# Kernel optimization log

Measured on AMD Instinct MI355X. Metric: run time of the kernel, lower is better.

The kernel has to match this reference:

```python
import jax, jax.numpy as jnp
import numpy as np

IMAGE_SIZE = (1024, 1024)
STRIDE = 16
RATIOS = (0.5, 1.0, 2.0)
SCALES = (8, 16, 32)
NUM_PRE_NMS = 6000
NUM_POST_NMS = 300
NMS_THRESH = 0.7
FEATURE_DEPTH = 512
RPN_DEPTH = 512
NUM_ANCHOR = len(RATIOS) * len(SCALES)


def _generate_anchors():
    # Faithful replication of RPN.__generate_anchors__ (numpy, at trace time).
    yloc = np.arange(STRIDE / 2, IMAGE_SIZE[0], STRIDE).astype(int)
    xloc = np.arange(STRIDE / 2, IMAGE_SIZE[1], STRIDE).astype(int)
    ctrs = np.array(np.meshgrid(xloc, yloc)).T.reshape(-1, 2)
    dims = [[STRIDE * s * np.sqrt(r), STRIDE * s * np.sqrt(1.0 / r)] for s in SCALES for r in RATIOS]
    blocks = []
    for d in dims:
        d = np.asarray(d)
        blocks.append(np.concatenate([ctrs - 0.5 * d, ctrs + 0.5 * d], axis=1))
    return np.concatenate(blocks, axis=0).astype(np.float32)  # (K*H*W, 4)

ANCHORS = _generate_anchors()


def conv2d(x, w, b, pad):
    y = jax.lax.conv_general_dilated(
        x, w, window_strides=(1, 1), padding=((pad, pad), (pad, pad)),
        dimension_numbers=('NCHW', 'OIHW', 'NCHW'))
    return y + b[None, :, None, None]


def nms_single(boxes, scores):
    # boxes: (A,4) yxyx, scores: (A,). Greedy NMS, jit-compatible.
    sc, idx = jax.lax.top_k(scores, NUM_PRE_NMS)
    b = boxes[idx]  # (P,4)
    y1, x1, y2, x2 = b[:, 0], b[:, 1], b[:, 2], b[:, 3]
    areas = (y2 - y1) * (x2 - x1)

    def body(i, carry):
        s, picked = carry
        j = jnp.argmax(s)
        picked = picked.at[i].set(j)
        bb = b[j]
        yy1 = jnp.maximum(bb[0], y1)
        xx1 = jnp.maximum(bb[1], x1)
        yy2 = jnp.minimum(bb[2], y2)
        xx2 = jnp.minimum(bb[3], x2)
        inter = jnp.maximum(yy2 - yy1, 0.0) * jnp.maximum(xx2 - xx1, 0.0)
        iou = inter / (areas[j] + areas - inter + 1e-9)
        s = jnp.where(iou >= NMS_THRESH, -jnp.inf, s)  # suppresses j itself (iou=1)
        return (s, picked)

    _, picked = jax.lax.fori_loop(0, NUM_POST_NMS, body, (sc, jnp.zeros((NUM_POST_NMS,), jnp.int32)))
    return b[picked]  # (POST, 4)


def rpn_forward(features, conv_w, conv_b, cls_w, cls_b, bbox_w, bbox_b):
    B, C, H, W = features.shape
    rpn = jax.nn.relu(conv2d(features, conv_w, conv_b, 1))
    # Objectness
    cls = conv2d(rpn, cls_w, cls_b, 0)  # (B, 2K, H, W)
    score = jnp.transpose(cls, (0, 2, 3, 1)).reshape(B, H, W, NUM_ANCHOR, 2)
    prob = jax.nn.softmax(score, axis=-1)[..., 1].reshape(B, -1)  # (B, A)
    score = score.reshape(B, -1, 2)
    tgt = conv2d(rpn, bbox_w, bbox_b, 0)  # (B, 4K, H, W)
    tgt = jnp.transpose(tgt, (0, 2, 3, 1)).reshape(B, -1, 4)
    # Decode targets against anchors (targets2box): (dy,dx,dh,dw) vs centre/hw anchors
    a = jnp.asarray(ANCHORS)
    ah = a[:, 2] - a[:, 0]
    aw = a[:, 3] - a[:, 1]
    acy = a[:, 0] + 0.5 * ah
    acx = a[:, 1] + 0.5 * aw
    dy, dx, dh, dw = tgt[..., 0], tgt[..., 1], tgt[..., 2], tgt[..., 3]
    pcy = acy + dy * ah
    pcx = acx + dx * aw
    ph = ah * jnp.exp(dh)
    pw = aw * jnp.exp(dw)
    boxes = jnp.stack([pcy - 0.5 * ph, pcx - 0.5 * pw, pcy + 0.5 * ph, pcx + 0.5 * pw], axis=-1)
    lim = jnp.array([IMAGE_SIZE[0] - 1, IMAGE_SIZE[1] - 1, IMAGE_SIZE[0] - 1, IMAGE_SIZE[1] - 1], boxes.dtype)
    boxes = jnp.clip(boxes, 0.0, lim)
    top = jax.vmap(nms_single)(boxes, prob)  # (B, POST, 4)
    return jnp.floor(top), score, tgt


def setup_inputs() -> dict:
    key = jax.random.key(0)
    ks = jax.random.split(key, 7)
    B, H, W = 8, IMAGE_SIZE[0] // STRIDE, IMAGE_SIZE[1] // STRIDE
    std = 0.01  # normal_init(mean=0, std=0.01) convention for RPN heads
    return {
        'features': jax.random.normal(ks[0], (B, FEATURE_DEPTH, H, W), jnp.float32),
        'conv_w': std * jax.random.normal(ks[1], (RPN_DEPTH, FEATURE_DEPTH, 3, 3), jnp.float32),
        'conv_b': jnp.zeros((RPN_DEPTH,), jnp.float32),
        'cls_w': std * jax.random.normal(ks[2], (NUM_ANCHOR * 2, RPN_DEPTH, 1, 1), jnp.float32),
        'cls_b': jnp.zeros((NUM_ANCHOR * 2,), jnp.float32),
        'bbox_w': std * jax.random.normal(ks[3], (NUM_ANCHOR * 4, RPN_DEPTH, 1, 1), jnp.float32),
        'bbox_b': jnp.zeros((NUM_ANCHOR * 4,), jnp.float32),
    }


def reference(features, conv_w, conv_b, cls_w, cls_b, bbox_w, bbox_b):
    return rpn_forward(features, conv_w, conv_b, cls_w, cls_b, bbox_w, bbox_b)
```

## Files before the change

### kernel.cpp

```cpp
#include <hip/hip_runtime.h>
#include <math.h>
#include <stdint.h>

typedef unsigned long long u64;

#define NANCH 36864
#define PRE_NMS 6000
#define POST_NMS 300

#define OFF_WT    0ull
#define OFF_KEYS  9437184ull
#define OFF_BOX   11796480ull
#define OFF_CAND  16515072ull
#define OFF_META  17039360ull
#define OFF_RPN   17039488ull

#define SCORE_OFF 9600u
#define TGT_OFF   599424u

__global__ void wt_kernel(const float* __restrict__ w, float* __restrict__ wt) {
    int idx = blockIdx.x * 256 + threadIdx.x;
    if (idx >= 9 * 512 * 512) return;
    int co = idx & 511;
    int ci = (idx >> 9) & 511;
    int tap = idx >> 18;
    wt[idx] = w[(size_t)(co * 512 + ci) * 9 + tap];
}

#define FS_CI6 432
#define FS_TOT6 3456
#define WS64 4608

__global__ __launch_bounds__(256, 2) void conv64(const float* __restrict__ F,
                                                 const float* __restrict__ Wt,
                                                 const float* __restrict__ bias,
                                                 float* __restrict__ rpn,
                                                 int b_base) {
    __shared__ __align__(16) float Fs[2][FS_TOT6];
    __shared__ __align__(16) float Ws[2][WS64];
    int t = threadIdx.x;
    int cg = t >> 5;
    int pg = t & 31;
    int rp = pg >> 4;
    int x0 = (pg & 15) << 2;
    int y0 = blockIdx.x << 2;
    int co0 = blockIdx.y * 64;
    int bl = blockIdx.z;
    const float* Fb = F + (size_t)(b_base + bl) * 512 * 4096;

    int rmap[6]; int nv = 0;
#pragma unroll
    for (int rr = 0; rr < 6; ++rr) {
        int gy = y0 + rr - 1;
        if (gy >= 0 && gy < 64) rmap[nv++] = rr;
    }
    int nF = (8 * 16) * nv;
    int fG[3], fL[3]; bool fV[3];
#pragma unroll
    for (int k = 0; k < 3; ++k) {
        int item = t + (k << 8);
        bool ok = item < nF;
        fV[k] = ok;
        int per_ci = nv << 4;
        int ci = ok ? (item / per_ci) : 0;
        int rem = item - ci * per_ci;
        if (!ok) rem = 0;
        int rv = rem >> 4;
        int f4 = rem & 15;
        int rr = rmap[rv];
        int gy = y0 + rr - 1;
        fG[k] = ci * 4096 + gy * 64 + (f4 << 2);
        fL[k] = ci * FS_CI6 + rr * 72 + 1 + (f4 << 2);
    }
    int wG[5], wL[5]; bool wV[5];
#pragma unroll
    for (int k = 0; k < 5; ++k) {
        int i4 = t + (k << 8);
        bool ok = i4 < 1152;
        wV[k] = ok;
        int idx = ok ? (i4 << 2) : 0;
        int ci = idx / 576;
        int rem = idx - ci * 576;
        int tap = rem >> 6;
        int co = rem & 63;
        wG[k] = tap * (512 * 512) + ci * 512 + co;
        wL[k] = idx;
    }
    float4 z4 = make_float4(0.f, 0.f, 0.f, 0.f);
    for (int i = t; i < (2 * FS_TOT6) / 4; i += 256) ((float4*)Fs)[i] = z4;

    float acc[8][2][4];
#pragma unroll
    for (int c2 = 0; c2 < 8; ++c2)
#pragma unroll
        for (int r = 0; r < 2; ++r)
#pragma unroll
            for (int j = 0; j < 4; ++j) acc[c2][r][j] = 0.f;

    float4 fQ[3], wQ[5];
#pragma unroll
    for (int k = 0; k < 3; ++k) fQ[k] = fV[k] ? *(const float4*)&Fb[fG[k]] : z4;
#pragma unroll
    for (int k = 0; k < 5; ++k) wQ[k] = wV[k] ? *(const float4*)&Wt[co0 + wG[k]] : z4;
#pragma unroll
    for (int k = 0; k < 3; ++k)
        if (fV[k]) {
            float* p = &Fs[0][fL[k]];
            p[0] = fQ[k].x; p[1] = fQ[k].y; p[2] = fQ[k].z; p[3] = fQ[k].w;
        }
#pragma unroll
    for (int k = 0; k < 5; ++k)
        if (wV[k]) *(float4*)&Ws[0][wL[k]] = wQ[k];
    {
        const float* Fn = Fb + 8 * 4096;
        const float* Wn = Wt + 8 * 512 + co0;
#pragma unroll
        for (int k = 0; k < 3; ++k) fQ[k] = fV[k] ? *(const float4*)&Fn[fG[k]] : z4;
#pragma unroll
        for (int k = 0; k < 5; ++k) wQ[k] = wV[k] ? *(const float4*)&Wn[wG[k]] : z4;
    }
    for (int c = 0; c < 64; ++c) {
        int cur = c & 1;
        int alt = cur ^ 1;
        __syncthreads();
        if (c + 1 < 64) {
#pragma unroll
            for (int k = 0; k < 3; ++k)
                if (fV[k]) {
                    float* p = &Fs[alt][fL[k]];
                    p[0] = fQ[k].x; p[1] = fQ[k].y; p[2] = fQ[k].z; p[3] = fQ[k].w;
                }
#pragma unroll
            for (int k = 0; k < 5; ++k)
                if (wV[k]) *(float4*)&Ws[alt][wL[k]] = wQ[k];
        }
        if (c + 2 < 64) {
            const float* Fn = Fb + (size_t)(c + 2) * 8 * 4096;
            const float* Wn = Wt + (size_t)(c + 2) * 8 * 512 + co0;
#pragma unroll
            for (int k = 0; k < 3; ++k) fQ[k] = fV[k] ? *(const float4*)&Fn[fG[k]] : z4;
#pragma unroll
            for (int k = 0; k < 5; ++k) wQ[k] = wV[k] ? *(const float4*)&Wn[wG[k]] : z4;
        }
#pragma unroll 1
        for (int ci = 0; ci < 8; ++ci) {
            float vv[4][6];
#pragma unroll
            for (int r2 = 0; r2 < 4; ++r2) {
                int base = ci * FS_CI6 + ((rp << 1) + r2) * 72 + x0;
                float4 a4 = *(float4*)&Fs[cur][base];
                float2 a2 = *(float2*)&Fs[cur][base + 4];
                vv[r2][0] = a4.x; vv[r2][1] = a4.y; vv[r2][2] = a4.z;
                vv[r2][3] = a4.w; vv[r2][4] = a2.x; vv[r2][5] = a2.y;
            }
#pragma unroll
            for (int tap = 0; tap < 9; ++tap) {
                int dy = tap / 3;
                int dx = tap % 3;
                int wb = ci * 576 + tap * 64 + cg * 8;
                float4 wa = *(float4*)&Ws[cur][wb];
                float4 wbv = *(float4*)&Ws[cur][wb + 4];
                float wv[8] = {wa.x, wa.y, wa.z, wa.w, wbv.x, wbv.y, wbv.z, wbv.w};
#pragma unroll
                for (int c2 = 0; c2 < 8; ++c2)
#pragma unroll
                    for (int r = 0; r < 2; ++r)
#pragma unroll
                        for (int j = 0; j < 4; ++j)
                            acc[c2][r][j] += wv[c2] * vv[r + dy][j + dx];
            }
        }
    }
#pragma unroll
    for (int c2 = 0; c2 < 8; ++c2) {
        int co = co0 + cg * 8 + c2;
        float bs = bias[co];
#pragma unroll
        for (int r = 0; r < 2; ++r) {
            int ry = y0 + (rp << 1) + r;
            float4 o;
            o.x = fmaxf(acc[c2][r][0] + bs, 0.f);
            o.y = fmaxf(acc[c2][r][1] + bs, 0.f);
            o.z = fmaxf(acc[c2][r][2] + bs, 0.f);
            o.w = fmaxf(acc[c2][r][3] + bs, 0.f);
            *(float4*)&rpn[(size_t)(bl * 512 + co) * 4096 + ry * 64 + x0] = o;
        }
    }
}

__global__ __launch_bounds__(512) void heads_lds(const float* __restrict__ rpn,
                                                 const float* __restrict__ cls_w,
                                                 const float* __restrict__ cls_b,
                                                 const float* __restrict__ bbox_w,
                                                 const float* __restrict__ bbox_b,
                                                 float* __restrict__ out,
                                                 u64* __restrict__ keys,
                                                 int b_base) {
    __shared__ float rT[64][64];
    __shared__ float wT[54][64];
    __shared__ float outS[54][64];
    int t = threadIdx.x;
    int px = t & 63;
    int g = t >> 6;
    int y = blockIdx.x;
    int bl = blockIdx.y;
    int b = b_base + bl;
    int nch = (g < 6) ? 7 : 6;

    float acc[7];
#pragma unroll
    for (int m = 0; m < 7; ++m) acc[m] = 0.f;

    for (int c8 = 0; c8 < 8; ++c8) {
#pragma unroll
        for (int i = 0; i < 2; ++i) {
            int f4 = t + (i << 9);
            int ci = f4 >> 4;
            int c4 = (f4 & 15) << 2;
            *(float4*)&rT[ci][c4] =
                *(const float4*)&rpn[((size_t)(bl * 512 + c8 * 64 + ci)) * 4096 + y * 64 + c4];
        }
#pragma unroll
        for (int i = 0; i < 2; ++i) {
            int f4 = t + (i << 9);
            if (f4 < 864) {
                int ch = f4 >> 4;
                int c4 = (f4 & 15) << 2;
                const float* src = (ch < 18)
                                       ? &cls_w[(size_t)ch * 512 + c8 * 64 + c4]
                                       : &bbox_w[(size_t)(ch - 18) * 512 + c8 * 64 + c4];
                *(float4*)&wT[ch][c4] = *(const float4*)src;
            }
        }
        __syncthreads();
        for (int ci = 0; ci < 64; ++ci) {
            float rv = rT[ci][px];
#pragma unroll
            for (int m = 0; m < 7; ++m) {
                if (m < nch) acc[m] += wT[g + (m << 3)][ci] * rv;
            }
        }
        __syncthreads();
    }
#pragma unroll
    for (int m = 0; m < 7; ++m) {
        if (m < nch) {
            int ch = g + (m << 3);
            float bs = (ch < 18) ? cls_b[ch] : bbox_b[ch - 18];
            outS[ch][px] = acc[m] + bs;
        }
    }
    __syncthreads();

    for (int fl = t; fl < 54 * 64; fl += 512) {
        int ch = fl >> 6;
        int p2 = fl & 63;
        float v = outS[ch][p2];
        size_t i0 = (size_t)(y * 64 + p2) * 9;
        if (ch < 18) {
            out[SCORE_OFF + ((size_t)b * NANCH + i0 + (ch >> 1)) * 2 + (ch & 1)] = v;
        } else {
            int c2 = ch - 18;
            out[TGT_OFF + ((size_t)b * NANCH + i0 + (c2 >> 2)) * 4 + (c2 & 3)] = v;
        }
    }
    for (int fl = t; fl < 9 * 64; fl += 512) {
        int a = fl >> 6;
        int p2 = fl & 63;
        float s0 = outS[a * 2][p2];
        float s1 = outS[a * 2 + 1][p2];
        float mm = fmaxf(s0, s1);
        float e0 = expf(s0 - mm);
        float e1 = expf(s1 - mm);
        float pr = e1 / (e0 + e1);
        int idx = (y * 64 + p2) * 9 + a;
        keys[(size_t)b * NANCH + idx] =
            ((u64)__float_as_uint(pr) << 32) | (u64)(0xFFFFFFFFu - (unsigned)idx);
    }
}

__global__ void box_kernel(const float* __restrict__ out, float* __restrict__ box) {
    int b = blockIdx.y;
    int i = blockIdx.x * 256 + threadIdx.x;
    const float* tg = &out[TGT_OFF + ((size_t)b * NANCH + i) * 4];
    float dyv = tg[0], dxv = tg[1], dhv = tg[2], dwv = tg[3];
    int dim = i >> 12, rem = i & 4095;
    double cxd = (double)(8 + 16 * (rem >> 6));
    double cyd = (double)(8 + 16 * (rem & 63));
    const double sca[3] = {8.0, 16.0, 32.0};
    const double rat[3] = {0.5, 1.0, 2.0};
    double sc = sca[dim / 3], ra = rat[dim % 3];
    double d0 = 16.0 * sc * sqrt(ra);
    double d1 = 16.0 * sc * sqrt(1.0 / ra);
    float a0 = (float)(cxd - 0.5 * d0);
    float a1 = (float)(cyd - 0.5 * d1);
    float a2 = (float)(cxd + 0.5 * d0);
    float a3 = (float)(cyd + 0.5 * d1);
    float ah = __fsub_rn(a2, a0), aw = __fsub_rn(a3, a1);
    float acy = __fadd_rn(a0, __fmul_rn(0.5f, ah));
    float acx = __fadd_rn(a1, __fmul_rn(0.5f, aw));
    float pcy = __fadd_rn(acy, __fmul_rn(dyv, ah));
    float pcx = __fadd_rn(acx, __fmul_rn(dxv, aw));
    float ph = __fmul_rn(ah, expf(dhv));
    float pw = __fmul_rn(aw, expf(dwv));
    float q0 = fminf(fmaxf(__fsub_rn(pcy, __fmul_rn(0.5f, ph)), 0.f), 1023.f);
    float q1 = fminf(fmaxf(__fsub_rn(pcx, __fmul_rn(0.5f, pw)), 0.f), 1023.f);
    float q2 = fminf(fmaxf(__fadd_rn(pcy, __fmul_rn(0.5f, ph)), 0.f), 1023.f);
    float q3 = fminf(fmaxf(__fadd_rn(pcx, __fmul_rn(0.5f, pw)), 0.f), 1023.f);
    *(float4*)&box[((size_t)b * NANCH + i) * 4] = make_float4(q0, q1, q2, q3);
}

__global__ __launch_bounds__(256) void select_kernel(const u64* __restrict__ keys,
                                                     u64* __restrict__ metaT,
                                                     unsigned* __restrict__ ctr) {
    __shared__ unsigned hist[256];
    __shared__ u64 sh_prefix;
    __shared__ unsigned sh_r;
    int b = blockIdx.x, t = threadIdx.x;
    if (t == 0) { sh_prefix = 0ull; sh_r = PRE_NMS; }
    __syncthreads();
    for (int round = 0; round < 8; ++round) {
        int shift = 56 - 8 * round;
        hist[t] = 0u;
        __syncthreads();
        u64 prefix = sh_prefix;
        for (int i = t; i < NANCH; i += 256) {
            u64 k = keys[(size_t)b * NANCH + i];
            bool ok = (round == 0) || ((k >> (shift + 8)) == prefix);
            if (ok) atomicAdd(&hist[(unsigned)(k >> shift) & 255u], 1u);
        }
        __syncthreads();
        if (t == 0) {
            unsigned r = sh_r, acc = 0;
            int digit = 0;
            for (int bin = 255; bin >= 0; --bin) {
                unsigned c = hist[bin];
                if (acc + c >= r) { digit = bin; sh_r = r - acc; break; }
                acc += c;
            }
            sh_prefix = (prefix << 8) | (u64)digit;
        }
        __syncthreads();
    }
    if (t == 0) {
        metaT[b] = sh_prefix;
        ctr[b] = 0u;
    }
}

__global__ void gather_kernel(const u64* __restrict__ keys, const u64* __restrict__ metaT,
                              unsigned* __restrict__ ctr, u64* __restrict__ candK) {
    int b = blockIdx.y;
    int i = blockIdx.x * 256 + threadIdx.x;
    u64 T = metaT[b];
    u64 k = keys[(size_t)b * NANCH + i];
    if (k >= T) {
        unsigned pos = atomicAdd(&ctr[b], 1u);
        if (pos < 8192u) candK[(size_t)b * 8192 + pos] = k;
    }
}

__global__ __launch_bounds__(512) void sortc_kernel(u64* __restrict__ candK) {
    __shared__ u64 K[8192];
    int b = blockIdx.x, t = threadIdx.x;
    for (int i = t; i < 8192; i += 512)
        K[i] = (i < PRE_NMS) ? candK[(size_t)b * 8192 + i] : 0ull;
    __syncthreads();
    for (int k = 2; k <= 8192; k <<= 1) {
        for (int j = k >> 1; j > 0; j >>= 1) {
            for (int i = t; i < 8192; i += 512) {
                int l = i ^ j;
                if (l > i) {
                    u64 a = K[i], c = K[l];
                    bool up = ((i & k) == 0);
                    bool sw = up ? (a < c) : (a > c);
                    if (sw) { K[i] = c; K[l] = a; }
                }
            }
            __syncthreads();
        }
    }
    for (int i = t; i < 8192; i += 512)
        candK[(size_t)b * 8192 + i] = K[i];
}

__global__ __launch_bounds__(256) void nms_scan(const u64* __restrict__ candK,
                                                const float* __restrict__ box,
                                                float* __restrict__ out_top) {
    __shared__ float kb0[POST_NMS], kb1[POST_NMS], kb2[POST_NMS], kb3[POST_NMS],
        kar[POST_NMS];
    __shared__ u64 mask[4];
    __shared__ float cand0[4];
    int b = blockIdx.x, t = threadIdx.x;
    int w = t >> 6, lane = t & 63;

    float c0[24], c1[24], c2[24], c3[24], ar[24];
    bool alv[24];
#pragma unroll
    for (int m = 0; m < 24; ++m) {
        int q = m * 256 + t;
        u64 kk = (q < PRE_NMS) ? candK[(size_t)b * 8192 + q] : 0ull;
        alv[m] = (kk != 0ull);
        if (alv[m]) {
            unsigned idx = 0xFFFFFFFFu - (unsigned)(kk & 0xFFFFFFFFull);
            const float* bp = &box[((size_t)b * NANCH + idx) * 4];
            c0[m] = bp[0]; c1[m] = bp[1]; c2[m] = bp[2]; c3[m] = bp[3];
        } else {
            c0[m] = c1[m] = c2[m] = c3[m] = 0.f;
        }
        ar[m] = __fmul_rn(__fsub_rn(c2[m], c0[m]), __fsub_rn(c3[m], c1[m]));
    }
    if (t == 0) { cand0[0] = c0[0]; cand0[1] = c1[0]; cand0[2] = c2[0]; cand0[3] = c3[0]; }

    int K = 0;
    bool done = false;
    for (int m = 0; m < 24 && !done; ++m) {
        bool a = alv[m];
        float C0 = c0[m], C1 = c1[m], C2 = c2[m], C3 = c3[m], AR = ar[m];
        for (int k = 0; k < K; ++k) {
            float yy1 = fmaxf(kb0[k], C0);
            float xx1 = fmaxf(kb1[k], C1);
            float yy2 = fminf(kb2[k], C2);
            float xx2 = fminf(kb3[k], C3);
            float inter = __fmul_rn(fmaxf(__fsub_rn(yy2, yy1), 0.f),
                                    fmaxf(__fsub_rn(xx2, xx1), 0.f));
            float denom = __fadd_rn(__fsub_rn(__fadd_rn(kar[k], AR), inter), 1e-9f);
            if (__fdiv_rn(inter, denom) >= 0.7f) a = false;
        }
        __syncthreads();
        u64 bal = __ballot(a);
        if (lane == 0) mask[w] = bal;
        __syncthreads();
        while (true) {
            int L = -1;
#pragma unroll
            for (int ww = 0; ww < 4; ++ww)
                if (L < 0 && mask[ww] != 0ull) L = ww * 64 + (__ffsll(mask[ww]) - 1);
            if (L < 0) break;
            if (t == L) {
                kb0[K] = C0; kb1[K] = C1; kb2[K] = C2; kb3[K] = C3; kar[K] = AR;
            }
            __syncthreads();
            float P0 = kb0[K], P1 = kb1[K], P2 = kb2[K], P3 = kb3[K], AP = kar[K];
            if (a) {
                float yy1 = fmaxf(P0, C0);
                float xx1 = fmaxf(P1, C1);
                float yy2 = fminf(P2, C2);
                float xx2 = fminf(P3, C3);
                float inter = __fmul_rn(fmaxf(__fsub_rn(yy2, yy1), 0.f),
                                        fmaxf(__fsub_rn(xx2, xx1), 0.f));
                float denom = __fadd_rn(__fsub_rn(__fadd_rn(AP, AR), inter), 1e-9f);
                if (__fdiv_rn(inter, denom) >= 0.7f) a = false;
            }
            K++;
            if (K == POST_NMS) done = true;
            u64 bal2 = __ballot(a);
            if (lane == 0) mask[w] = bal2;
            __syncthreads();
            if (done) break;
        }
    }
    __syncthreads();
    for (int i = t; i < POST_NMS; i += 256) {
        float o0, o1, o2, o3;
        if (i < K) { o0 = kb0[i]; o1 = kb1[i]; o2 = kb2[i]; o3 = kb3[i]; }
        else       { o0 = cand0[0]; o1 = cand0[1]; o2 = cand0[2]; o3 = cand0[3]; }
        float* o = out_top + ((size_t)b * POST_NMS + i) * 4;
        o[0] = floorf(o0); o[1] = floorf(o1); o[2] = floorf(o2); o[3] = floorf(o3);
    }
}

extern "C" void kernel_launch(void* const* d_in, const int* in_sizes, int n_in,
                              void* d_out, int out_size, void* d_ws, size_t ws_size,
                              hipStream_t stream) {
    (void)in_sizes; (void)n_in; (void)out_size; (void)ws_size;
    const float* features = (const float*)d_in[0];
    const float* conv_w = (const float*)d_in[1];
    const float* conv_b = (const float*)d_in[2];
    const float* cls_w = (const float*)d_in[3];
    const float* cls_b = (const float*)d_in[4];
    const float* bbox_w = (const float*)d_in[5];
    const float* bbox_b = (const float*)d_in[6];
    float* out = (float*)d_out;
    char* ws = (char*)d_ws;

    float* Wt = (float*)(ws + OFF_WT);
    u64* keys = (u64*)(ws + OFF_KEYS);
    float* box = (float*)(ws + OFF_BOX);
    u64* candK = (u64*)(ws + OFF_CAND);
    u64* metaT = (u64*)(ws + OFF_META);
    unsigned* ctr = (unsigned*)(ws + OFF_META + 64);
    float* rpn = (float*)(ws + OFF_RPN);

    wt_kernel<<<9216, 256, 0, stream>>>(conv_w, Wt);
    for (int h = 0; h < 2; ++h) {
        int b_base = h * 4;
        conv64<<<dim3(16, 8, 4), 256, 0, stream>>>(features, Wt, conv_b, rpn, b_base);
        heads_lds<<<dim3(64, 4), 512, 0, stream>>>(rpn, cls_w, cls_b, bbox_w, bbox_b,
                                                   out, keys, b_base);
    }
    box_kernel<<<dim3(144, 8), 256, 0, stream>>>(out, box);
    select_kernel<<<8, 256, 0, stream>>>(keys, metaT, ctr);
    gather_kernel<<<dim3(144, 8), 256, 0, stream>>>(keys, metaT, ctr, candK);
    sortc_kernel<<<8, 512, 0, stream>>>(candK);
    nms_scan<<<8, 256, 0, stream>>>(candK, box, out);
}
```

Before: 2.520 ms.

## Single-buffer conv LDS and launch all batches at once when workspace allows

The conv kernel drops its double-buffered shared memory for one buffer, with a register prefetch of the next chunk stored after a second barrier. This halves LDS use and removes the launch_bounds hint, so more blocks may fit per CU. When the workspace is large enough, the conv and heads kernels now run over all 8 images in one launch instead of two halves, giving a larger grid and fewer launches. The cost is an extra barrier per channel chunk and less overlap between loads and compute.

```diff
diff --git a/kernel.cpp b/kernel.cpp
--- a/kernel.cpp
+++ b/kernel.cpp
@@ -14,6 +14,8 @@
 #define OFF_CAND  16515072ull
 #define OFF_META  17039360ull
 #define OFF_RPN   17039488ull
+#define IMG_BYTES 8388608ull
+#define WS_NEED8  84148352ull
 
 #define SCORE_OFF 9600u
 #define TGT_OFF   599424u
@@ -31,13 +33,13 @@
 #define FS_TOT6 3456
 #define WS64 4608
 
-__global__ __launch_bounds__(256, 2) void conv64(const float* __restrict__ F,
-                                                 const float* __restrict__ Wt,
-                                                 const float* __restrict__ bias,
-                                                 float* __restrict__ rpn,
-                                                 int b_base) {
-    __shared__ __align__(16) float Fs[2][FS_TOT6];
-    __shared__ __align__(16) float Ws[2][WS64];
+__global__ void conv64s(const float* __restrict__ F,
+                        const float* __restrict__ Wt,
+                        const float* __restrict__ bias,
+                        float* __restrict__ rpn,
+                        int b_base) {
+    __shared__ __align__(16) float Fs[FS_TOT6];
+    __shared__ __align__(16) float Ws[WS64];
     int t = threadIdx.x;
     int cg = t >> 5;
     int pg = t & 31;
@@ -87,7 +89,7 @@
         wL[k] = idx;
     }
     float4 z4 = make_float4(0.f, 0.f, 0.f, 0.f);
-    for (int i = t; i < (2 * FS_TOT6) / 4; i += 256) ((float4*)Fs)[i] = z4;
+    for (int i = t; i < FS_TOT6 / 4; i += 256) ((float4*)Fs)[i] = z4;
 
     float acc[8][2][4];
 #pragma unroll
@@ -105,38 +107,18 @@
 #pragma unroll
     for (int k = 0; k < 3; ++k)
         if (fV[k]) {
-            float* p = &Fs[0][fL[k]];
+            float* p = &Fs[fL[k]];
             p[0] = fQ[k].x; p[1] = fQ[k].y; p[2] = fQ[k].z; p[3] = fQ[k].w;
         }
 #pragma unroll
     for (int k = 0; k < 5; ++k)
-        if (wV[k]) *(float4*)&Ws[0][wL[k]] = wQ[k];
-    {
-        const float* Fn = Fb + 8 * 4096;
-        const float* Wn = Wt + 8 * 512 + co0;
-#pragma unroll
-        for (int k = 0; k < 3; ++k) fQ[k] = fV[k] ? *(const float4*)&Fn[fG[k]] : z4;
-#pragma unroll
-        for (int k = 0; k < 5; ++k) wQ[k] = wV[k] ? *(const float4*)&Wn[wG[k]] : z4;
-    }
+        if (wV[k]) *(float4*)&Ws[wL[k]] = wQ[k];
+
     for (int c = 0; c < 64; ++c) {
-        int cur = c & 1;
-        int alt = cur ^ 1;
         __syncthreads();
         if (c + 1 < 64) {
-#pragma unroll
-            for (int k = 0; k < 3; ++k)
-                if (fV[k]) {
-                    float* p = &Fs[alt][fL[k]];
-                    p[0] = fQ[k].x; p[1] = fQ[k].y; p[2] = fQ[k].z; p[3] = fQ[k].w;
-                }
-#pragma unroll
-            for (int k = 0; k < 5; ++k)
-                if (wV[k]) *(float4*)&Ws[alt][wL[k]] = wQ[k];
-        }
-        if (c + 2 < 64) {
-            const float* Fn = Fb + (size_t)(c + 2) * 8 * 4096;
-            const float* Wn = Wt + (size_t)(c + 2) * 8 * 512 + co0;
+            const float* Fn = Fb + (size_t)(c + 1) * 8 * 4096;
+            const float* Wn = Wt + (size_t)(c + 1) * 8 * 512 + co0;
 #pragma unroll
             for (int k = 0; k < 3; ++k) fQ[k] = fV[k] ? *(const float4*)&Fn[fG[k]] : z4;
 #pragma unroll
@@ -148,8 +130,8 @@
 #pragma unroll
             for (int r2 = 0; r2 < 4; ++r2) {
                 int base = ci * FS_CI6 + ((rp << 1) + r2) * 72 + x0;
-                float4 a4 = *(float4*)&Fs[cur][base];
-                float2 a2 = *(float2*)&Fs[cur][base + 4];
+                float4 a4 = *(float4*)&Fs[base];
+                float2 a2 = *(float2*)&Fs[base + 4];
                 vv[r2][0] = a4.x; vv[r2][1] = a4.y; vv[r2][2] = a4.z;
                 vv[r2][3] = a4.w; vv[r2][4] = a2.x; vv[r2][5] = a2.y;
             }
@@ -158,8 +140,8 @@
                 int dy = tap / 3;
                 int dx = tap % 3;
                 int wb = ci * 576 + tap * 64 + cg * 8;
-                float4 wa = *(float4*)&Ws[cur][wb];
-                float4 wbv = *(float4*)&Ws[cur][wb + 4];
+                float4 wa = *(float4*)&Ws[wb];
+                float4 wbv = *(float4*)&Ws[wb + 4];
                 float wv[8] = {wa.x, wa.y, wa.z, wa.w, wbv.x, wbv.y, wbv.z, wbv.w};
 #pragma unroll
                 for (int c2 = 0; c2 < 8; ++c2)
@@ -169,6 +151,18 @@
                         for (int j = 0; j < 4; ++j)
                             acc[c2][r][j] += wv[c2] * vv[r + dy][j + dx];
             }
+        }
+        __syncthreads();
+        if (c + 1 < 64) {
+#pragma unroll
+            for (int k = 0; k < 3; ++k)
+                if (fV[k]) {
+                    float* p = &Fs[fL[k]];
+                    p[0] = fQ[k].x; p[1] = fQ[k].y; p[2] = fQ[k].z; p[3] = fQ[k].w;
+                }
+#pragma unroll
+            for (int k = 0; k < 5; ++k)
+                if (wV[k]) *(float4*)&Ws[wL[k]] = wQ[k];
         }
     }
 #pragma unroll
@@ -473,7 +467,7 @@
 extern "C" void kernel_launch(void* const* d_in, const int* in_sizes, int n_in,
                               void* d_out, int out_size, void* d_ws, size_t ws_size,
                               hipStream_t stream) {
-    (void)in_sizes; (void)n_in; (void)out_size; (void)ws_size;
+    (void)in_sizes; (void)n_in; (void)out_size;
     const float* features = (const float*)d_in[0];
     const float* conv_w = (const float*)d_in[1];
     const float* conv_b = (const float*)d_in[2];
@@ -493,11 +487,17 @@
     float* rpn = (float*)(ws + OFF_RPN);
 
     wt_kernel<<<9216, 256, 0, stream>>>(conv_w, Wt);
-    for (int h = 0; h < 2; ++h) {
-        int b_base = h * 4;
-        conv64<<<dim3(16, 8, 4), 256, 0, stream>>>(features, Wt, conv_b, rpn, b_base);
-        heads_lds<<<dim3(64, 4), 512, 0, stream>>>(rpn, cls_w, cls_b, bbox_w, bbox_b,
-                                                   out, keys, b_base);
+    if (ws_size >= WS_NEED8) {
+        conv64s<<<dim3(16, 8, 8), 256, 0, stream>>>(features, Wt, conv_b, rpn, 0);
+        heads_lds<<<dim3(64, 8), 512, 0, stream>>>(rpn, cls_w, cls_b, bbox_w, bbox_b,
+                                                   out, keys, 0);
+    } else {
+        for (int h = 0; h < 2; ++h) {
+            int b_base = h * 4;
+            conv64s<<<dim3(16, 8, 4), 256, 0, stream>>>(features, Wt, conv_b, rpn, b_base);
+            heads_lds<<<dim3(64, 4), 512, 0, stream>>>(rpn, cls_w, cls_b, bbox_w, bbox_b,
+                                                       out, keys, b_base);
+        }
     }
     box_kernel<<<dim3(144, 8), 256, 0, stream>>>(out, box);
     select_kernel<<<8, 256, 0, stream>>>(keys, metaT, ctr);
```

After: 4.061 ms. 1.61x slower.
